# Kernel tuning notes

Hardware: AMD Instinct MI355X
Metric: run time of the kernel (lower is better)

## Reference

```python
import jax, jax.numpy as jnp
import numpy as np

N = 100000   # nodes per graph
E = 1600000  # edges (avg degree 16)
B = 2        # num_graph (batch)
F_IN = 116   # num_input
EMB = 12     # embedding dim
H = 128      # hidden_size


def setup_inputs() -> dict:
    key = jax.random.key(0)
    ks = jax.random.split(key, 8)
    node = jax.random.normal(ks[0], (B, N, F_IN), dtype=jnp.float32)
    node_type = jax.random.randint(ks[1], (N,), 0, 8, dtype=jnp.int32)
    edge_index = jax.random.randint(ks[2], (2, E), 0, N, dtype=jnp.int32)
    embed = jax.random.normal(ks[3], (8, EMB), dtype=jnp.float32)
    d1 = F_IN + EMB
    W1 = jax.random.normal(ks[4], (d1, H), dtype=jnp.float32) / np.sqrt(d1)
    b1 = jnp.zeros((H,), dtype=jnp.float32)
    W2 = jax.random.normal(ks[5], (H, H), dtype=jnp.float32) / np.sqrt(H)
    b2 = jnp.zeros((H,), dtype=jnp.float32)
    return {"node": node, "node_type": node_type, "edge_index": edge_index,
            "embed": embed, "W1": W1, "b1": b1, "W2": W2, "b2": b2}


def _gcn_conv(x, src, dst, W, b):
    """PyG GCNConv: symmetric norm with self-loops, linear (no lin bias), bias after agg.
    x: [B, N, F]; src/dst: [E] int; W: [F, H]; b: [H]."""
    n = x.shape[1]
    # degree over (A + I), computed on destination nodes
    deg = jnp.zeros((n,), x.dtype).at[dst].add(1.0) + 1.0
    dis = jax.lax.rsqrt(deg)  # deg^{-1/2}
    xw = jnp.einsum('bnf,fh->bnh', x, W)          # [B, N, H]
    norm = dis[src] * dis[dst]                    # [E]
    msgs = xw[:, src, :] * norm[None, :, None]    # [B, E, H]
    agg = jax.vmap(lambda m: jax.ops.segment_sum(m, dst, num_segments=n))(msgs)
    agg = agg + xw * (dis * dis)[None, :, None]   # self-loop contribution
    return agg + b


def reference(node, node_type, edge_index, embed, W1, b1, W2, b2):
    src, dst = edge_index[0], edge_index[1]
    emb = embed[node_type]                                      # [N, EMB]
    b = node.shape[0]
    emb_b = jnp.broadcast_to(emb[None], (b,) + emb.shape)       # repeat over batch
    x = jnp.concatenate([node, emb_b], axis=2)                  # [B, N, F_IN+EMB]
    x = jax.nn.relu(_gcn_conv(x, src, dst, W1, b1))
    # F.dropout in eval mode is identity
    x = _gcn_conv(x, src, dst, W2, b2)
    return jnp.mean(x, axis=1)                                  # [B, H]
```

## Files before the change

kernel.cpp:

```cpp
#include <hip/hip_runtime.h>
#include <stdint.h>

typedef unsigned int uint32;
typedef unsigned short ushort16;
typedef __attribute__((ext_vector_type(8))) short bf16x8;
typedef __attribute__((ext_vector_type(4))) float f32x4;
typedef __attribute__((ext_vector_type(2))) float f32x2;

#define F_IN 116
#define HID  128
#define EMBD 12
#define IDX24 0x00FFFFFFu
#define BCAP 4608
#define PCAP 8448

__device__ __forceinline__ ushort16 f2bf(float f) {
    uint32 x = __float_as_uint(f);
    uint32 r = (x + 0x7fffu + ((x >> 16) & 1u)) >> 16;
    return (ushort16)r;
}

__global__ void k_init(int* __restrict__ bcurD, int* __restrict__ bcurS,
                       float* __restrict__ partial, uint32* __restrict__ xwzrow,
                       int* __restrict__ csrz, int NZ, int K) {
    int i = blockIdx.x * 256 + threadIdx.x;
    if (i < K) { bcurD[i] = i * BCAP; bcurS[i] = i * BCAP; }
    if (blockIdx.x == 0) {
        partial[threadIdx.x] = 0.f;
        if (threadIdx.x < 64) xwzrow[threadIdx.x] = 0u;
        if (threadIdx.x < 16) csrz[threadIdx.x] = NZ;
    }
}

__global__ void k_prepB(const float* __restrict__ W1, ushort16* __restrict__ W1s) {
    int tid = blockIdx.x * blockDim.x + threadIdx.x;
    if (tid >= 2048) return;
    int q = tid & 3, n = (tid >> 2) & 15, t = (tid >> 6) & 7, kc = (tid >> 9) & 3;
    int chunk = ((kc * 8 + t) * 64 + n * 4 + q);
#pragma unroll
    for (int j = 0; j < 8; ++j) {
        int k = kc * 32 + q * 8 + j;
        W1s[chunk * 8 + j] = f2bf(W1[k * HID + t * 16 + n]);
    }
}

__global__ __launch_bounds__(256) void k_bin(
    const int* __restrict__ src, const int* __restrict__ dst,
    int* __restrict__ bcurD, int* __restrict__ bcurS,
    uint32* __restrict__ ebufD, uint32* __restrict__ ebufS, int E) {
    __shared__ int lhD[512], lbD[512], lhS[512], lbS[512];
    const int tid = threadIdx.x;
    const int e0 = blockIdx.x * 8192;
    const int eend = min(e0 + 8192, E);
    for (int i = tid; i < 512; i += 256) { lhD[i] = 0; lhS[i] = 0; }
    __syncthreads();
    for (int e = e0 + tid; e < eend; e += 256) {
        atomicAdd(&lhD[dst[e] >> 8], 1);
        atomicAdd(&lhS[src[e] >> 8], 1);
    }
    __syncthreads();
    const int rot = (blockIdx.x * 277) & 511;
#pragma unroll
    for (int i = 0; i < 2; ++i) {
        int k = (rot + tid + i * 256) & 511;
        int c = lhD[k]; lbD[k] = c ? atomicAdd(&bcurD[k], c) : 0; lhD[k] = 0;
        int d = lhS[k]; lbS[k] = d ? atomicAdd(&bcurS[k], d) : 0; lhS[k] = 0;
    }
    __syncthreads();
    for (int e = e0 + tid; e < eend; e += 256) {
        int s = src[e], d = dst[e];
        int bkD = d >> 8;
        int p = lbD[bkD] + atomicAdd(&lhD[bkD], 1);
        if (p < (bkD + 1) * BCAP) ebufD[p] = ((uint32)(d & 255) << 24) | (uint32)s;
        int bkS = s >> 8;
        int p2 = lbS[bkS] + atomicAdd(&lhS[bkS], 1);
        if (p2 < (bkS + 1) * BCAP) ebufS[p2] = ((uint32)(s & 255) << 24) | (uint32)d;
    }
}

__global__ __launch_bounds__(256) void k_csr(
    const uint32* __restrict__ ebufD, const int* __restrict__ bcurD,
    int4* __restrict__ meta, float* __restrict__ dis,
    int* __restrict__ csr, int N, int ZROW) {
    __shared__ int cnt[256];
    __shared__ int cur[256];
    __shared__ int lst[256];
    __shared__ int ps[256];
    const int b = blockIdx.x, tid = threadIdx.x;
    const int r0 = b * BCAP;
    const int r1 = min(bcurD[b], r0 + BCAP);
    cnt[tid] = 0;
    __syncthreads();
    for (int p = r0 + tid; p < r1; p += 256)
        atomicAdd(&cnt[ebufD[p] >> 24], 1);
    __syncthreads();
    const int pl = (cnt[tid] + 15) & ~15;
    ps[tid] = pl;
    __syncthreads();
    for (int off = 1; off < 256; off <<= 1) {
        int t = (tid >= off) ? ps[tid - off] : 0;
        __syncthreads();
        ps[tid] += t;
        __syncthreads();
    }
    const int start = b * PCAP + ps[tid] - pl;
    lst[tid] = start;
    cur[tid] = start;
    const int n = (b << 8) + tid;
    float dl = rsqrtf(1.0f + (float)cnt[tid]);
    if (n < N) {
        dis[n] = dl;
        meta[n] = make_int4(start, pl >> 4, __float_as_int(dl), 0);
    }
    __syncthreads();
    for (int p = r0 + tid; p < r1; p += 256) {
        uint32 v = ebufD[p];
        csr[atomicAdd(&cur[v >> 24], 1)] = (int)(v & IDX24);
    }
    __syncthreads();
    {
        int end = lst[tid] + pl;
        for (int p = cur[tid]; p < end; ++p) csr[p] = ZROW;
    }
}

__global__ __launch_bounds__(256) void k_souts(
    const uint32* __restrict__ ebufS, const int* __restrict__ bcurS,
    const float* __restrict__ dis, int4* __restrict__ meta, int N) {
    __shared__ float lso[256];
    const int b = blockIdx.x, tid = threadIdx.x;
    const int r0 = b * BCAP;
    const int r1 = min(bcurS[b], r0 + BCAP);
    lso[tid] = 0.f;
    __syncthreads();
    for (int p = r0 + tid; p < r1; p += 256) {
        uint32 v = ebufS[p];
        atomicAdd(&lso[v >> 24], dis[v & IDX24]);
    }
    __syncthreads();
    int n = (b << 8) + tid;
    if (n < N) meta[n].w = __float_as_int(lso[tid]);
}

__global__ __launch_bounds__(256, 4) void k_gemm(
    const float* __restrict__ node, const ushort16* __restrict__ W1s,
    const int* __restrict__ ntype, const float* __restrict__ embed,
    const float* __restrict__ dis, uint32* __restrict__ xw8, int N, int M)
{
    __shared__ ushort16 ldsA[4 * 4 * 64 * 8];
    __shared__ float ldis[32];
    const int tid = threadIdx.x;
    const int row0 = blockIdx.x * 64;

    if (tid < 32) {
        int n = (row0 >> 1) + tid;
        ldis[tid] = (n < N) ? dis[n] : 0.f;
    }

    const int g = tid & 31;
    const int kc0 = g >> 3, q0 = (g >> 1) & 3, half = g & 1;
#pragma unroll
    for (int j = 0; j < 8; ++j) {
        int r = (tid >> 5) + j * 8;
        int m = row0 + r;
        int n = m >> 1, b = m & 1;
        float4 v = make_float4(0.f, 0.f, 0.f, 0.f);
        if (n < N) {
            if (g < 29) v = *(const float4*)(node + ((size_t)b * N + n) * F_IN + g * 4);
            else        v = *(const float4*)(embed + ntype[n] * EMBD + (g - 29) * 4);
        }
        uint32 u0 = (uint32)f2bf(v.x) | ((uint32)f2bf(v.y) << 16);
        uint32 u1 = (uint32)f2bf(v.z) | ((uint32)f2bf(v.w) << 16);
        int mt = r >> 4, mloc = r & 15;
        int chunk = (mt * 4 + kc0) * 64 + mloc * 4 + q0;
        *(uint2*)&ldsA[chunk * 8 + half * 4] = make_uint2(u0, u1);
    }
    __syncthreads();

    const int lane = tid & 63;
    const int w = tid >> 6;
    const int fragsel = (lane & 15) * 4 + (lane >> 4);

    f32x4 acc[8];
#pragma unroll
    for (int ct = 0; ct < 8; ++ct) acc[ct] = (f32x4){0.f, 0.f, 0.f, 0.f};

#pragma unroll
    for (int kc = 0; kc < 4; ++kc) {
        bf16x8 bfr = *(const bf16x8*)&ldsA[(((w * 4 + kc) * 64) + fragsel) * 8];
#pragma unroll
        for (int ct = 0; ct < 8; ++ct) {
            bf16x8 afr = *(const bf16x8*)&W1s[(((kc * 8 + ct) * 64) + fragsel) * 8];
            acc[ct] = __builtin_amdgcn_mfma_f32_16x16x32_bf16(afr, bfr, acc[ct], 0, 0, 0);
        }
    }

    const int row = lane & 15, q = lane >> 4;
    int m = row0 + w * 16 + row;
    if (m < M) {
        float dn = ldis[(w * 16 + row) >> 1];
        uint32* rowp = xw8 + (size_t)m * 32;
#pragma unroll
        for (int ct = 0; ct < 8; ++ct) {
            f32x4 a = acc[ct];
            int u = __builtin_amdgcn_cvt_pk_fp8_f32(a[0] * dn, a[1] * dn, 0, false);
            u = __builtin_amdgcn_cvt_pk_fp8_f32(a[2] * dn, a[3] * dn, u, true);
            rowp[ct * 4 + q] = (uint32)u;
        }
    }
}

__global__ __launch_bounds__(256) void k_gather(
    const uint32* __restrict__ xw8, const int* __restrict__ csr,
    const int4* __restrict__ meta, const float* __restrict__ b1,
    float* __restrict__ partial, int N, int ZT)
{
    __shared__ float sm[4][256];
    const int tid  = threadIdx.x;
    const int lane = tid & 63;
    const int wid  = tid >> 6;
    const int wv = (blockIdx.x * blockDim.x + tid) >> 6;
    const int nw = (gridDim.x * blockDim.x) >> 6;
    const int c0 = (lane & 31) * 4;
    const int slot = (lane >> 5) * HID + c0;
    const float bb0 = b1[c0], bb1 = b1[c0 + 1], bb2 = b1[c0 + 2], bb3 = b1[c0 + 3];

    float p0 = 0.f, p1 = 0.f, p2 = 0.f, p3 = 0.f;

    for (int n = wv * 2; n < N; n += nw * 2) {
        const int ns = __builtin_amdgcn_readfirstlane(n);
        const int has2 = (ns + 1 < N);
        const int4 m1 = meta[ns];
        const int4 m2 = has2 ? meta[ns + 1] : make_int4(0, 0, 0, 0);
        const int st1 = m1.x, c1 = m1.y;
        const float dn1 = __int_as_float(m1.z), so1 = __int_as_float(m1.w);
        const int st2 = m2.x, c2 = m2.y;
        const float dn2 = __int_as_float(m2.z), so2 = __int_as_float(m2.w);

        uint32 sv1 = xw8[(size_t)ns * 64 + lane];
        uint32 sv2 = has2 ? xw8[((size_t)ns + 1) * 64 + lane] : 0u;
        f32x2 lo1 = __builtin_amdgcn_cvt_pk_f32_fp8(sv1, false);
        f32x2 hi1 = __builtin_amdgcn_cvt_pk_f32_fp8(sv1, true);
        f32x2 lo2 = __builtin_amdgcn_cvt_pk_f32_fp8(sv2, false);
        f32x2 hi2 = __builtin_amdgcn_cvt_pk_f32_fp8(sv2, true);
        float a10 = lo1.x, a11 = lo1.y, a12 = hi1.x, a13 = hi1.y;
        float a20 = lo2.x, a21 = lo2.y, a22 = hi2.x, a23 = hi2.y;

        int o1 = (c1 > 0) ? st1 : ZT;
        int o2 = (c2 > 0) ? st2 : ZT;
        int4 A0 = *(const int4*)&csr[o1];      int4 A1 = *(const int4*)&csr[o1 + 4];
        int4 A2 = *(const int4*)&csr[o1 + 8];  int4 A3 = *(const int4*)&csr[o1 + 12];
        int4 B0 = *(const int4*)&csr[o2];      int4 B1 = *(const int4*)&csr[o2 + 4];
        int4 B2 = *(const int4*)&csr[o2 + 8];  int4 B3 = *(const int4*)&csr[o2 + 12];

        const int jm = max(c1, c2);
        for (int j = 0; j < jm; ++j) {
            uint32 w1[16], w2[16];
            w1[0]  = xw8[(size_t)A0.x * 64 + lane];
            w1[1]  = xw8[(size_t)A0.y * 64 + lane];
            w1[2]  = xw8[(size_t)A0.z * 64 + lane];
            w1[3]  = xw8[(size_t)A0.w * 64 + lane];
            w1[4]  = xw8[(size_t)A1.x * 64 + lane];
            w1[5]  = xw8[(size_t)A1.y * 64 + lane];
            w1[6]  = xw8[(size_t)A1.z * 64 + lane];
            w1[7]  = xw8[(size_t)A1.w * 64 + lane];
            w1[8]  = xw8[(size_t)A2.x * 64 + lane];
            w1[9]  = xw8[(size_t)A2.y * 64 + lane];
            w1[10] = xw8[(size_t)A2.z * 64 + lane];
            w1[11] = xw8[(size_t)A2.w * 64 + lane];
            w1[12] = xw8[(size_t)A3.x * 64 + lane];
            w1[13] = xw8[(size_t)A3.y * 64 + lane];
            w1[14] = xw8[(size_t)A3.z * 64 + lane];
            w1[15] = xw8[(size_t)A3.w * 64 + lane];
            w2[0]  = xw8[(size_t)B0.x * 64 + lane];
            w2[1]  = xw8[(size_t)B0.y * 64 + lane];
            w2[2]  = xw8[(size_t)B0.z * 64 + lane];
            w2[3]  = xw8[(size_t)B0.w * 64 + lane];
            w2[4]  = xw8[(size_t)B1.x * 64 + lane];
            w2[5]  = xw8[(size_t)B1.y * 64 + lane];
            w2[6]  = xw8[(size_t)B1.z * 64 + lane];
            w2[7]  = xw8[(size_t)B1.w * 64 + lane];
            w2[8]  = xw8[(size_t)B2.x * 64 + lane];
            w2[9]  = xw8[(size_t)B2.y * 64 + lane];
            w2[10] = xw8[(size_t)B2.z * 64 + lane];
            w2[11] = xw8[(size_t)B2.w * 64 + lane];
            w2[12] = xw8[(size_t)B3.x * 64 + lane];
            w2[13] = xw8[(size_t)B3.y * 64 + lane];
            w2[14] = xw8[(size_t)B3.z * 64 + lane];
            w2[15] = xw8[(size_t)B3.w * 64 + lane];

            const int j1 = j + 1;
            o1 = (j1 < c1) ? st1 + j1 * 16 : ZT;
            o2 = (j1 < c2) ? st2 + j1 * 16 : ZT;
            A0 = *(const int4*)&csr[o1];      A1 = *(const int4*)&csr[o1 + 4];
            A2 = *(const int4*)&csr[o1 + 8];  A3 = *(const int4*)&csr[o1 + 12];
            B0 = *(const int4*)&csr[o2];      B1 = *(const int4*)&csr[o2 + 4];
            B2 = *(const int4*)&csr[o2 + 8];  B3 = *(const int4*)&csr[o2 + 12];

#pragma unroll
            for (int k = 0; k < 16; ++k) {
                f32x2 lo = __builtin_amdgcn_cvt_pk_f32_fp8(w1[k], false);
                f32x2 hi = __builtin_amdgcn_cvt_pk_f32_fp8(w1[k], true);
                a10 += lo.x; a11 += lo.y; a12 += hi.x; a13 += hi.y;
            }
#pragma unroll
            for (int k = 0; k < 16; ++k) {
                f32x2 lo = __builtin_amdgcn_cvt_pk_f32_fp8(w2[k], false);
                f32x2 hi = __builtin_amdgcn_cvt_pk_f32_fp8(w2[k], true);
                a20 += lo.x; a21 += lo.y; a22 += hi.x; a23 += hi.y;
            }
        }

        float cf1 = dn1 * (dn1 + so1);
        p0 = fmaf(cf1, fmaxf(fmaf(dn1, a10, bb0), 0.f), p0);
        p1 = fmaf(cf1, fmaxf(fmaf(dn1, a11, bb1), 0.f), p1);
        p2 = fmaf(cf1, fmaxf(fmaf(dn1, a12, bb2), 0.f), p2);
        p3 = fmaf(cf1, fmaxf(fmaf(dn1, a13, bb3), 0.f), p3);
        if (has2) {
            float cf2 = dn2 * (dn2 + so2);
            p0 = fmaf(cf2, fmaxf(fmaf(dn2, a20, bb0), 0.f), p0);
            p1 = fmaf(cf2, fmaxf(fmaf(dn2, a21, bb1), 0.f), p1);
            p2 = fmaf(cf2, fmaxf(fmaf(dn2, a22, bb2), 0.f), p2);
            p3 = fmaf(cf2, fmaxf(fmaf(dn2, a23, bb3), 0.f), p3);
        }
    }

    *(float4*)&sm[wid][slot] = make_float4(p0, p1, p2, p3);
    __syncthreads();
    if (tid < 256) {
        float s = sm[0][tid] + sm[1][tid] + sm[2][tid] + sm[3][tid];
        atomicAdd(&partial[tid], s);
    }
}

__global__ void k_final(const float* __restrict__ partial, const float* __restrict__ W2,
                        const float* __restrict__ b2, float* __restrict__ out, float invN) {
    int tid = threadIdx.x;
    int b = tid >> 7, h = tid & 127;
    float acc = 0.f;
#pragma unroll 8
    for (int k = 0; k < HID; ++k)
        acc += partial[b * HID + k] * W2[k * HID + h];
    out[tid] = acc * invN + b2[h];
}

extern "C" void kernel_launch(void* const* d_in, const int* in_sizes, int n_in,
                              void* d_out, int out_size, void* d_ws, size_t ws_size,
                              hipStream_t stream) {
    const float* node  = (const float*)d_in[0];
    const int*   ntype = (const int*)d_in[1];
    const int*   eidx  = (const int*)d_in[2];
    const float* embed = (const float*)d_in[3];
    const float* W1    = (const float*)d_in[4];
    const float* b1    = (const float*)d_in[5];
    const float* W2    = (const float*)d_in[6];
    const float* b2    = (const float*)d_in[7];
    float* out = (float*)d_out;

    const int N  = in_sizes[1];
    const int E  = in_sizes[2] / 2;
    const int B  = in_sizes[0] / (N * F_IN);
    const int M  = B * N;
    const int K  = (N + 255) >> 8;

    const int* src = eidx;
    const int* dst = eidx + E;

    char* ws = (char*)d_ws;
    size_t off = 0;
    auto alloc = [&](size_t bytes) -> void* {
        void* p = ws + off;
        off += (bytes + 255) & ~(size_t)255;
        return p;
    };
    uint32*   xw8     = (uint32*)alloc((size_t)(M + 2) * 128);
    int*      csr     = (int*)alloc(((size_t)K * PCAP + 16) * sizeof(int));
    uint32*   ebufD   = (uint32*)alloc((size_t)K * BCAP * sizeof(uint32));
    uint32*   ebufS   = (uint32*)alloc((size_t)K * BCAP * sizeof(uint32));
    int4*     meta    = (int4*)alloc((size_t)N * sizeof(int4));
    float*    dis     = (float*)alloc((size_t)N * sizeof(float));
    ushort16* W1s     = (ushort16*)alloc(4 * 8 * 64 * 8 * sizeof(ushort16));
    int*      bcurD   = (int*)alloc((size_t)K * sizeof(int));
    int*      bcurS   = (int*)alloc((size_t)K * sizeof(int));
    float*    partial = (float*)alloc(2 * HID * sizeof(float));

    const int ZT = K * PCAP;

    k_init<<<(K + 255) / 256, 256, 0, stream>>>(bcurD, bcurS, partial, xw8 + (size_t)N * 64,
                                                csr + (size_t)ZT, N, K);
    k_prepB<<<8, 256, 0, stream>>>(W1, W1s);
    k_bin<<<(E + 8191) / 8192, 256, 0, stream>>>(src, dst, bcurD, bcurS, ebufD, ebufS, E);
    k_csr<<<K, 256, 0, stream>>>(ebufD, bcurD, meta, dis, csr, N, N);
    k_souts<<<K, 256, 0, stream>>>(ebufS, bcurS, dis, meta, N);
    k_gemm<<<(M + 63) / 64, 256, 0, stream>>>(node, W1s, ntype, embed, dis, xw8, N, M);
    k_gather<<<2048, 256, 0, stream>>>(xw8, csr, meta, b1, partial, N, ZT);
    k_final<<<1, 256, 0, stream>>>(partial, W2, b2, out, 1.0f / (float)N);
}
```

Baseline: 374.9 us.

## Merge setup kernels, halve bin chunk, split gather into two launches

Folds k_init and k_prepB into a single k_setup launch to save one kernel launch. k_bin now handles 4096 edges per block instead of 8192, giving it twice as many blocks. k_gather gets a launch-bounds occupancy hint and a compiler memory barrier between the index loads and the conversion loop. It also now runs as two 1536-block launches over the two halves of the node range, presumably to improve cache locality. Splitting the gather adds a launch, and the barrier may constrain instruction scheduling.

```diff
diff --git a/kernel.cpp b/kernel.cpp
--- a/kernel.cpp
+++ b/kernel.cpp
@@ -20,27 +20,25 @@
     return (ushort16)r;
 }
 
-__global__ void k_init(int* __restrict__ bcurD, int* __restrict__ bcurS,
-                       float* __restrict__ partial, uint32* __restrict__ xwzrow,
-                       int* __restrict__ csrz, int NZ, int K) {
-    int i = blockIdx.x * 256 + threadIdx.x;
-    if (i < K) { bcurD[i] = i * BCAP; bcurS[i] = i * BCAP; }
+__global__ void k_setup(const float* __restrict__ W1, ushort16* __restrict__ W1s,
+                        int* __restrict__ bcurD, int* __restrict__ bcurS,
+                        float* __restrict__ partial, uint32* __restrict__ xwzrow,
+                        int* __restrict__ csrz, int N, int K) {
+    int tid = blockIdx.x * 256 + threadIdx.x;
+    if (tid < K) { bcurD[tid] = tid * BCAP; bcurS[tid] = tid * BCAP; }
     if (blockIdx.x == 0) {
         partial[threadIdx.x] = 0.f;
         if (threadIdx.x < 64) xwzrow[threadIdx.x] = 0u;
-        if (threadIdx.x < 16) csrz[threadIdx.x] = NZ;
-    }
-}
-
-__global__ void k_prepB(const float* __restrict__ W1, ushort16* __restrict__ W1s) {
-    int tid = blockIdx.x * blockDim.x + threadIdx.x;
-    if (tid >= 2048) return;
-    int q = tid & 3, n = (tid >> 2) & 15, t = (tid >> 6) & 7, kc = (tid >> 9) & 3;
-    int chunk = ((kc * 8 + t) * 64 + n * 4 + q);
-#pragma unroll
-    for (int j = 0; j < 8; ++j) {
-        int k = kc * 32 + q * 8 + j;
-        W1s[chunk * 8 + j] = f2bf(W1[k * HID + t * 16 + n]);
+        if (threadIdx.x < 16) csrz[threadIdx.x] = N;
+    }
+    if (tid < 2048) {
+        int q = tid & 3, n = (tid >> 2) & 15, t = (tid >> 6) & 7, kc = (tid >> 9) & 3;
+        int chunk = ((kc * 8 + t) * 64 + n * 4 + q);
+#pragma unroll
+        for (int j = 0; j < 8; ++j) {
+            int k = kc * 32 + q * 8 + j;
+            W1s[chunk * 8 + j] = f2bf(W1[k * HID + t * 16 + n]);
+        }
     }
 }
 
@@ -50,8 +48,8 @@
     uint32* __restrict__ ebufD, uint32* __restrict__ ebufS, int E) {
     __shared__ int lhD[512], lbD[512], lhS[512], lbS[512];
     const int tid = threadIdx.x;
-    const int e0 = blockIdx.x * 8192;
-    const int eend = min(e0 + 8192, E);
+    const int e0 = blockIdx.x * 4096;
+    const int eend = min(e0 + 4096, E);
     for (int i = tid; i < 512; i += 256) { lhD[i] = 0; lhS[i] = 0; }
     __syncthreads();
     for (int e = e0 + tid; e < eend; e += 256) {
@@ -210,10 +208,10 @@
     }
 }
 
-__global__ __launch_bounds__(256) void k_gather(
+__global__ __launch_bounds__(256, 4) void k_gather(
     const uint32* __restrict__ xw8, const int* __restrict__ csr,
     const int4* __restrict__ meta, const float* __restrict__ b1,
-    float* __restrict__ partial, int N, int ZT)
+    float* __restrict__ partial, int n0, int n1, int ZT)
 {
     __shared__ float sm[4][256];
     const int tid  = threadIdx.x;
@@ -227,9 +225,9 @@
 
     float p0 = 0.f, p1 = 0.f, p2 = 0.f, p3 = 0.f;
 
-    for (int n = wv * 2; n < N; n += nw * 2) {
+    for (int n = n0 + wv * 2; n < n1; n += nw * 2) {
         const int ns = __builtin_amdgcn_readfirstlane(n);
-        const int has2 = (ns + 1 < N);
+        const int has2 = (ns + 1 < n1);
         const int4 m1 = meta[ns];
         const int4 m2 = has2 ? meta[ns + 1] : make_int4(0, 0, 0, 0);
         const int st1 = m1.x, c1 = m1.y;
@@ -297,6 +295,8 @@
             B0 = *(const int4*)&csr[o2];      B1 = *(const int4*)&csr[o2 + 4];
             B2 = *(const int4*)&csr[o2 + 8];  B3 = *(const int4*)&csr[o2 + 12];
 
+            asm volatile("" ::: "memory");
+
 #pragma unroll
             for (int k = 0; k < 16; ++k) {
                 f32x2 lo = __builtin_amdgcn_cvt_pk_f32_fp8(w1[k], false);
@@ -385,14 +385,15 @@
     float*    partial = (float*)alloc(2 * HID * sizeof(float));
 
     const int ZT = K * PCAP;
-
-    k_init<<<(K + 255) / 256, 256, 0, stream>>>(bcurD, bcurS, partial, xw8 + (size_t)N * 64,
-                                                csr + (size_t)ZT, N, K);
-    k_prepB<<<8, 256, 0, stream>>>(W1, W1s);
-    k_bin<<<(E + 8191) / 8192, 256, 0, stream>>>(src, dst, bcurD, bcurS, ebufD, ebufS, E);
+    const int Nh = (N / 2 + 1) & ~1;
+
+    k_setup<<<8, 256, 0, stream>>>(W1, W1s, bcurD, bcurS, partial,
+                                   xw8 + (size_t)N * 64, csr + (size_t)ZT, N, K);
+    k_bin<<<(E + 4095) / 4096, 256, 0, stream>>>(src, dst, bcurD, bcurS, ebufD, ebufS, E);
     k_csr<<<K, 256, 0, stream>>>(ebufD, bcurD, meta, dis, csr, N, N);
     k_souts<<<K, 256, 0, stream>>>(ebufS, bcurS, dis, meta, N);
     k_gemm<<<(M + 63) / 64, 256, 0, stream>>>(node, W1s, ntype, embed, dis, xw8, N, M);
-    k_gather<<<2048, 256, 0, stream>>>(xw8, csr, meta, b1, partial, N, ZT);
+    k_gather<<<1536, 256, 0, stream>>>(xw8, csr, meta, b1, partial, 0, Nh, ZT);
+    k_gather<<<1536, 256, 0, stream>>>(xw8, csr, meta, b1, partial, Nh, N, ZT);
     k_final<<<1, 256, 0, stream>>>(partial, W2, b2, out, 1.0f / (float)N);
 }
```

Result: slower. 404.5 us (+7.9%).
